# Performance work log

Hardware: AMD Instinct MI355X
Metric: run time of the kernel (lower is better)

The kernel has to match this reference:

```python
import jax, jax.numpy as jnp
import numpy as np

B, S, D, H, F = 8, 1024, 1024, 16, 4096
DH = D // H
EPS = 1e-8
NEG_INF = -1e30


def setup_inputs() -> dict:
    key = jax.random.key(0)
    ks = jax.random.split(key, 12)
    x = jax.random.normal(ks[0], (B, S, D), jnp.float32)
    # variable valid lengths in [S//2, S]; True = keep (valid token)
    lengths = jax.random.randint(ks[1], (B,), S // 2, S + 1)
    src_key_padding_mask = jnp.arange(S)[None, :] < lengths[:, None]
    rel_pos_bias = 0.02 * jax.random.normal(ks[2], (1, H, S, S), jnp.float32)
    w = lambda k, sh, std: std * jax.random.normal(k, sh, jnp.float32)
    std = D ** -0.5
    return {
        'x': x,
        'src_key_padding_mask': src_key_padding_mask,
        'rel_pos_bias': rel_pos_bias,
        'Wq': w(ks[3], (D, D), std),
        'Wk': w(ks[4], (D, D), std),
        'Wv': w(ks[5], (D, D), std),
        'Wo': w(ks[6], (D, D), std),
        'g1': jnp.ones((D,), jnp.float32),
        'g2': jnp.ones((D,), jnp.float32),
        'W1': w(ks[7], (D, F), std),
        'b1': jnp.zeros((F,), jnp.float32),
        'W2': w(ks[8], (F, F and D), F ** -0.5),
        'b2': jnp.zeros((D,), jnp.float32),
    }


def rmsnorm(x, g):
    # x / sqrt(mean(x^2) + eps) * g   (no mean subtraction)
    ms = jnp.mean(x * x, axis=-1, keepdims=True)
    return x * jax.lax.rsqrt(ms + EPS) * g


def attention(h, kpm, rel_pos_bias, Wq, Wk, Wv, Wo):
    b, s, d = h.shape
    q = (h @ Wq).reshape(b, s, H, DH)
    k = (h @ Wk).reshape(b, s, H, DH)
    v = (h @ Wv).reshape(b, s, H, DH)
    scores = jnp.einsum('bqhd,bkhd->bhqk', q, k) / np.sqrt(DH)
    scores = scores + rel_pos_bias
    scores = jnp.where(kpm[:, None, None, :], scores, NEG_INF)
    attn = jax.nn.softmax(scores, axis=-1)
    out = jnp.einsum('bhqk,bkhd->bqhd', attn, v).reshape(b, s, d)
    return out @ Wo


def reference(x, src_key_padding_mask, rel_pos_bias,
              Wq, Wk, Wv, Wo, g1, g2, W1, b1, W2, b2):
    h = rmsnorm(x, g1)
    x = x + attention(h, src_key_padding_mask, rel_pos_bias, Wq, Wk, Wv, Wo)
    h = rmsnorm(x, g2)
    ff = jax.nn.relu(h @ W1 + b1) @ W2 + b2
    return x + ff
```

## Files before the change

kernel.cpp:

```cpp
#include <hip/hip_runtime.h>
#include <stdint.h>

typedef __bf16 bf16;
typedef __bf16 bf16x4 __attribute__((ext_vector_type(4)));
typedef __bf16 bf16x8 __attribute__((ext_vector_type(8)));
typedef float f32x4 __attribute__((ext_vector_type(4)));

constexpr int Bz = 8, S = 1024, D = 1024, NH = 16, DH = 64, F = 4096;

__device__ __forceinline__ bool is_f32(const uint16_t* dt) { return dt[0] == 0; }

__device__ __forceinline__ void ld4(const void* p, size_t idx, bool f32, float o[4]) {
  if (f32) {
    float4 v = *(const float4*)((const float*)p + idx);
    o[0] = v.x; o[1] = v.y; o[2] = v.z; o[3] = v.w;
  } else {
    bf16x4 v = *(const bf16x4*)((const bf16*)p + idx);
    o[0] = v[0]; o[1] = v[1]; o[2] = v[2]; o[3] = v[3];
  }
}

__device__ __forceinline__ float ld1(const void* p, size_t idx, bool f32) {
  return f32 ? ((const float*)p)[idx] : (float)((const bf16*)p)[idx];
}

__device__ __forceinline__ void gload_lds16(const bf16* g, bf16* l) {
  __builtin_amdgcn_global_load_lds(
      (const __attribute__((address_space(1))) void*)g,
      (__attribute__((address_space(3))) void*)l, 16, 0, 0);
}

__global__ void lengths_kernel(const unsigned char* __restrict__ mask,
                               int* __restrict__ lengths) {
  int b = blockIdx.x;
  int esz = (mask[1] == 1) ? 1 : ((mask[1] != 0) ? 2 : 4);
  int cnt = 0;
  for (int s = threadIdx.x; s < S; s += blockDim.x) {
    const unsigned char* p = mask + ((size_t)b * S + s) * esz;
    unsigned v = 0;
    for (int j = 0; j < esz; j++) v |= p[j];
    cnt += (v != 0) ? 1 : 0;
  }
#pragma unroll
  for (int m = 32; m >= 1; m >>= 1) cnt += __shfl_xor(cnt, m);
  __shared__ int sred[4];
  if ((threadIdx.x & 63) == 0) sred[threadIdx.x >> 6] = cnt;
  __syncthreads();
  if (threadIdx.x == 0) lengths[b] = sred[0] + sred[1] + sred[2] + sred[3];
}

__global__ void transpose_any(const void* __restrict__ src, bf16* __restrict__ dst,
                              int R, int C, const uint16_t* __restrict__ dt) {
  bool f32 = is_f32(dt);
  __shared__ bf16 tile[64][65];
  int c0 = blockIdx.x * 64, r0 = blockIdx.y * 64;
  int tx = threadIdx.x, ty = threadIdx.y;
#pragma unroll
  for (int i = 0; i < 4; i++) {
    int r = ty * 4 + i;
    float v[4];
    ld4(src, (size_t)(r0 + r) * C + c0 + tx * 4, f32, v);
#pragma unroll
    for (int j = 0; j < 4; j++) tile[r][tx * 4 + j] = (bf16)v[j];
  }
  __syncthreads();
#pragma unroll
  for (int i = 0; i < 4; i++) {
    int rr = ty * 4 + i;
    bf16x4 ov;
#pragma unroll
    for (int j = 0; j < 4; j++) ov[j] = tile[tx * 4 + j][rr];
    *(bf16x4*)(dst + (size_t)(c0 + rr) * R + r0 + tx * 4) = ov;
  }
}

__global__ void bias_cvt(const void* __restrict__ src, bf16* __restrict__ dst,
                         const uint16_t* __restrict__ dt) {
  bool f32 = is_f32(dt);
  size_t i = ((size_t)blockIdx.x * 256 + threadIdx.x) * 4;
  float v[4];
  ld4(src, i, f32, v);
  bf16x4 o;
#pragma unroll
  for (int j = 0; j < 4; j++) o[j] = (bf16)(v[j] * 1.4426950408889634f);
  *(bf16x4*)(dst + i) = o;
}

template <bool ADD>
__global__ void rmsnorm_kernel(const void* __restrict__ xv, const bf16* __restrict__ add,
                               const void* __restrict__ gv, bf16* __restrict__ y,
                               const uint16_t* __restrict__ dt) {
  bool f32 = is_f32(dt);
  int row = blockIdx.x, t = threadIdx.x;
  float xf[4];
  ld4(xv, (size_t)row * D + t * 4, f32, xf);
  if (ADD) {
    bf16x4 a = *(const bf16x4*)(add + (size_t)row * D + t * 4);
#pragma unroll
    for (int j = 0; j < 4; j++) xf[j] += (float)a[j];
  }
  float ss = xf[0] * xf[0] + xf[1] * xf[1] + xf[2] * xf[2] + xf[3] * xf[3];
#pragma unroll
  for (int m = 32; m >= 1; m >>= 1) ss += __shfl_xor(ss, m);
  __shared__ float sred[4];
  if ((t & 63) == 0) sred[t >> 6] = ss;
  __syncthreads();
  float tot = sred[0] + sred[1] + sred[2] + sred[3];
  float scale = rsqrtf(tot * (1.0f / D) + 1e-8f);
  float gf[4];
  ld4(gv, (size_t)t * 4, f32, gf);
  bf16x4 ov;
#pragma unroll
  for (int j = 0; j < 4; j++) ov[j] = (bf16)(xf[j] * scale * gf[j]);
  *(bf16x4*)(y + (size_t)row * D + t * 4) = ov;
}

template <bool BIAS, bool RELU, bool RES1, bool RES2, bool OUTEXT, bool VT>
__global__ void gemm_nt(const bf16* __restrict__ A, const bf16* __restrict__ Bt,
                        void* __restrict__ Cv, const void* __restrict__ biasv,
                        const void* __restrict__ res1, const bf16* __restrict__ res2,
                        int M, int N, int K, const uint16_t* __restrict__ dt) {
  bool f32 = is_f32(dt);
  __shared__ bf16 As[2 * 4096];
  __shared__ bf16 Bs[2 * 4096];
  const int tid = threadIdx.x, lane = tid & 63, w = tid >> 6;
  const int wm = w >> 1, wn = w & 1;
  const int lid = blockIdx.x;
  const int bm = ((lid & 7) << 3) + ((lid >> 3) & 7);
  const int bn = lid >> 6;
  const int quad = lane >> 4, c = lane & 15;

  f32x4 acc[4][4];
#pragma unroll
  for (int i = 0; i < 4; i++)
#pragma unroll
    for (int j = 0; j < 4; j++)
#pragma unroll
      for (int r = 0; r < 4; r++) acc[i][j][r] = 0.f;

  const bf16* gA = A + (size_t)(bm * 128 + w * 16 + (lane >> 2)) * K + (lane & 3) * 8;
  const bf16* gB = Bt + (size_t)(bn * 128 + w * 16 + (lane >> 2)) * K + (lane & 3) * 8;
  bf16* lA = As + w * 512;
  bf16* lB = Bs + w * 512;
  const size_t rstep = (size_t)64 * K;

  int aoff[4], boff[4];
#pragma unroll
  for (int i = 0; i < 4; i++) {
    aoff[i] = (wm * 64 + i * 16 + c) * 32 + quad * 8;
    boff[i] = (wn * 64 + i * 16 + c) * 32 + quad * 8;
  }

  for (int k0 = 0; k0 < K; k0 += 64) {
    __syncthreads();
#pragma unroll
    for (int p = 0; p < 2; p++) {
      gload_lds16(gA + p * 32, lA + p * 4096);
      gload_lds16(gA + p * 32 + rstep, lA + p * 4096 + 2048);
      gload_lds16(gB + p * 32, lB + p * 4096);
      gload_lds16(gB + p * 32 + rstep, lB + p * 4096 + 2048);
    }
    gA += 64;
    gB += 64;
    __syncthreads();
#pragma unroll
    for (int p = 0; p < 2; p++) {
      bf16x8 af[4], bfr[4];
#pragma unroll
      for (int i = 0; i < 4; i++) af[i] = *(const bf16x8*)(As + p * 4096 + aoff[i]);
#pragma unroll
      for (int i = 0; i < 4; i++) bfr[i] = *(const bf16x8*)(Bs + p * 4096 + boff[i]);
#pragma unroll
      for (int i = 0; i < 4; i++)
#pragma unroll
        for (int j = 0; j < 4; j++)
          acc[i][j] = __builtin_amdgcn_mfma_f32_16x16x32_bf16(af[i], bfr[j], acc[i][j], 0, 0, 0);
    }
  }

  const int m0 = bm * 128 + wm * 64, n0 = bn * 128 + wn * 64;
#pragma unroll
  for (int i = 0; i < 4; i++) {
#pragma unroll
    for (int j = 0; j < 4; j++) {
      int col = n0 + j * 16 + c;
      if (VT) {
        int row0 = m0 + i * 16 + quad * 4;
        int bb = row0 >> 10, s0 = row0 & 1023;
        int hh = col >> 6, dd = col & 63;
        bf16x4 ov;
#pragma unroll
        for (int r = 0; r < 4; r++) ov[r] = (bf16)acc[i][j][r];
        *(bf16x4*)((bf16*)Cv + ((size_t)((bb << 4) + hh) * 64 + dd) * 1024 + s0) = ov;
      } else {
        float bv = BIAS ? ld1(biasv, col, f32) : 0.f;
#pragma unroll
        for (int r = 0; r < 4; r++) {
          int row = m0 + i * 16 + quad * 4 + r;
          size_t idx = (size_t)row * N + col;
          float vv = acc[i][j][r] + bv;
          if (RELU) vv = fmaxf(vv, 0.f);
          if (RES1) vv += ld1(res1, idx, f32);
          if (RES2) vv += (float)res2[idx];
          if (OUTEXT && f32) ((float*)Cv)[idx] = vv;
          else ((bf16*)Cv)[idx] = (bf16)vv;
        }
      }
    }
  }
}

#define SYNC()                            \
  do {                                    \
    __builtin_amdgcn_sched_barrier(0);    \
    __builtin_amdgcn_s_barrier();         \
    __builtin_amdgcn_sched_barrier(0);    \
  } while (0)
#define VMW(n)                                              \
  do {                                                      \
    asm volatile("s_waitcnt vmcnt(" #n ")" ::: "memory");   \
    __builtin_amdgcn_sched_barrier(0);                      \
  } while (0)
#define STA_(nb, rowbase, kb)                                                  \
  do {                                                                         \
    gload_lds16(Ag + (size_t)(rowbase) * K + (kb), &Abuf[nb][(rowbase) * 64]); \
    gload_lds16(Ag + (size_t)((rowbase) + 8) * K + (kb),                       \
                &Abuf[nb][((rowbase) + 8) * 64]);                              \
  } while (0)
#define STB_(nb, rowbase, kb)                                                  \
  do {                                                                         \
    gload_lds16(Bg + (size_t)(rowbase) * K + (kb), &Bbuf[nb][(rowbase) * 64]); \
    gload_lds16(Bg + (size_t)((rowbase) + 8) * K + (kb),                       \
                &Bbuf[nb][((rowbase) + 8) * 64]);                              \
  } while (0)
#define RDA_(MQ, fr, bufsel)                                                        \
  do {                                                                              \
    _Pragma("unroll") for (int ii = 0; ii < 4; ii++) {                              \
      int arow = wm * 128 + ((MQ)*4 + ii) * 16 + c;                                 \
      fr[ii][0] = *(const bf16x8*)&Abuf[bufsel][arow * 64 + ((quad ^ sx) * 8)];     \
      fr[ii][1] = *(const bf16x8*)&Abuf[bufsel][arow * 64 + (((4 + quad) ^ sx) * 8)]; \
    }                                                                               \
  } while (0)
#define RDB_(NQ, fr, bufsel)                                                        \
  do {                                                                              \
    _Pragma("unroll") for (int jj = 0; jj < 2; jj++) {                              \
      int brow = wn * 64 + ((NQ)*2 + jj) * 16 + c;                                  \
      fr[jj][0] = *(const bf16x8*)&Bbuf[bufsel][brow * 64 + ((quad ^ sx) * 8)];     \
      fr[jj][1] = *(const bf16x8*)&Bbuf[bufsel][brow * 64 + (((4 + quad) ^ sx) * 8)]; \
    }                                                                               \
  } while (0)

template <int MQ, int NQ>
__device__ __forceinline__ void mm_phase(f32x4 (&acc)[8][4], const bf16x8 (&afr)[4][2],
                                         const bf16x8 (&bfr)[2][2]) {
#pragma unroll
  for (int ii = 0; ii < 4; ii++)
#pragma unroll
    for (int jj = 0; jj < 2; jj++) {
      acc[MQ * 4 + ii][NQ * 2 + jj] = __builtin_amdgcn_mfma_f32_16x16x32_bf16(
          afr[ii][0], bfr[jj][0], acc[MQ * 4 + ii][NQ * 2 + jj], 0, 0, 0);
      acc[MQ * 4 + ii][NQ * 2 + jj] = __builtin_amdgcn_mfma_f32_16x16x32_bf16(
          afr[ii][1], bfr[jj][1], acc[MQ * 4 + ii][NQ * 2 + jj], 0, 0, 0);
    }
}

template <bool BIAS, bool RELU>
__global__ void __launch_bounds__(512, 2) gemm256(
    const bf16* __restrict__ A, const bf16* __restrict__ Bt, bf16* __restrict__ C,
    const void* __restrict__ biasv, int N, int K, const uint16_t* __restrict__ dt) {
  bool f32 = is_f32(dt);
  __shared__ bf16 Abuf[2][256 * 64];
  __shared__ bf16 Bbuf[2][256 * 64];
  const int tid = threadIdx.x, lane = tid & 63, w = tid >> 6;
  const int wm = w >> 2, wn = w & 3;
  const int quad = lane >> 4, c = lane & 15;
  const int sx = c & 7;
  const int nbn = N >> 8;
  const int nwg = gridDim.x;
  const int sid = (blockIdx.x & 7) * (nwg >> 3) + (blockIdx.x >> 3);
  const int bm = sid / nbn, bn = sid % nbn;

  const int lrow = lane >> 3;
  const int lslot = ((lane & 7) ^ lrow) * 8;
  const bf16* Ag = A + (size_t)(bm * 256 + lrow) * K + lslot;
  const bf16* Bg = Bt + (size_t)(bn * 256 + lrow) * K + lslot;

  const int ra0 = wm * 128 + wn * 16;
  const int ra1 = ra0 + 64;
  const int rb0 = (wn >> 1) * 128 + (wn & 1) * 64 + wm * 16;
  const int rb1 = rb0 + 32;

  f32x4 acc[8][4];
#pragma unroll
  for (int i = 0; i < 8; i++)
#pragma unroll
    for (int j = 0; j < 4; j++)
#pragma unroll
      for (int r = 0; r < 4; r++) acc[i][j][r] = 0.f;

  const int nt = K >> 6;

  STA_(0, ra0, 0);
  STA_(0, ra1, 0);
  STB_(0, rb0, 0);
  STB_(0, rb1, 0);
  STA_(1, ra0, 64);
  VMW(2);
  SYNC();

  for (int t = 0; t < nt; ++t) {
    const int buf = t & 1, nb = buf ^ 1;
    const int kb1 = (t + 1) << 6, kb2 = (t + 2) << 6;
    const bool st1 = (t + 1 < nt), st2 = (t + 2 < nt);
    bf16x8 afr[4][2], bfr0[2][2], bfr1[2][2];
    RDA_(0, afr, buf);
    RDB_(0, bfr0, buf);
    if (st1) STA_(nb, ra1, kb1);
    SYNC();
    __builtin_amdgcn_s_setprio(1);
    mm_phase<0, 0>(acc, afr, bfr0);
    __builtin_amdgcn_s_setprio(0);
    VMW(2);
    SYNC();
    RDB_(1, bfr1, buf);
    if (st1) STB_(nb, rb0, kb1);
    SYNC();
    __builtin_amdgcn_s_setprio(1);
    mm_phase<0, 1>(acc, afr, bfr1);
    __builtin_amdgcn_s_setprio(0);
    SYNC();
    RDA_(1, afr, buf);
    if (st2) STA_(buf, ra0, kb2);
    SYNC();
    __builtin_amdgcn_s_setprio(1);
    mm_phase<1, 0>(acc, afr, bfr0);
    __builtin_amdgcn_s_setprio(0);
    SYNC();
    if (st1) STB_(nb, rb1, kb1);
    SYNC();
    __builtin_amdgcn_s_setprio(1);
    mm_phase<1, 1>(acc, afr, bfr1);
    __builtin_amdgcn_s_setprio(0);
    VMW(4);
    SYNC();
  }

  const int m0 = bm * 256 + wm * 128, n0 = bn * 256 + wn * 64;
#pragma unroll
  for (int fi = 0; fi < 8; fi++)
#pragma unroll
    for (int fj = 0; fj < 4; fj++) {
      int col = n0 + fj * 16 + c;
      float bv = BIAS ? ld1(biasv, col, f32) : 0.f;
#pragma unroll
      for (int r = 0; r < 4; r++) {
        int row = m0 + fi * 16 + quad * 4 + r;
        float vv = acc[fi][fj][r] + bv;
        if (RELU) vv = fmaxf(vv, 0.f);
        C[(size_t)row * N + col] = (bf16)vv;
      }
    }
}

__global__ void __launch_bounds__(256) attn_kernel(
    const bf16* __restrict__ qk, const bf16* __restrict__ vt,
    const bf16* __restrict__ bias, const int* __restrict__ lengths,
    bf16* __restrict__ out) {
  __shared__ bf16 QPs[64 * 72];
  __shared__ bf16 Ks[64][72];
  __shared__ bf16 Vs[64][72];
  const int tid = threadIdx.x, lane = tid & 63, w = tid >> 6;
  const int id = blockIdx.x;
  const int qt = id >> 7, b = (id >> 4) & 7, h = id & 15;
  const int len = lengths[b];
  const int quad = lane >> 4, c = lane & 15;
  const int r4 = tid >> 2, c4 = tid & 3;

  {
    size_t qrow = (size_t)(b * S + qt * 64 + r4) * 2048 + h * 64 + c4 * 8;
    *(bf16x8*)&QPs[r4 * 72 + c4 * 8] = *(const bf16x8*)&qk[qrow];
    *(bf16x8*)&QPs[r4 * 72 + 32 + c4 * 8] = *(const bf16x8*)&qk[qrow + 32];
  }
  __syncthreads();
  const bf16x8 a0 = *(const bf16x8*)&QPs[(w * 16 + c) * 72 + quad * 8];
  const bf16x8 a1 = *(const bf16x8*)&QPs[(w * 16 + c) * 72 + 32 + quad * 8];

  bf16* Pw = QPs + w * 16 * 72;
  const int xsw = (quad & 2) << 3;
  const int xsr = (c & 8) << 1;

  float l_[4] = {0.f, 0.f, 0.f, 0.f};
  f32x4 o[4];
#pragma unroll
  for (int ni = 0; ni < 4; ni++)
#pragma unroll
    for (int r = 0; r < 4; r++) o[ni][r] = 0.f;

  const bf16* bbp = bias + (size_t)h * S * S + (size_t)(qt * 64 + w * 16 + quad * 4) * S;
  const int nkt = (len + 63) >> 6;

  const size_t KSTEP = (size_t)64 * 2048;
  const bf16* gk = qk + (size_t)(b * S + r4) * 2048 + 1024 + h * 64 + c4 * 8;
  const bf16* gv = vt + ((size_t)((b * 16 + h) * 64 + r4)) * 1024 + c4 * 8;
  bf16x8 kr0 = *(const bf16x8*)gk;
  bf16x8 kr1 = *(const bf16x8*)(gk + 32);
  bf16x8 vr0 = *(const bf16x8*)gv;
  bf16x8 vr1 = *(const bf16x8*)(gv + 32);
  gk += KSTEP;
  gv += 64;

  for (int kt = 0; kt < nkt; kt++) {
    __syncthreads();
    *(bf16x8*)&Ks[r4][c4 * 8] = kr0;
    *(bf16x8*)&Ks[r4][32 + c4 * 8] = kr1;
    *(bf16x8*)&Vs[r4][c4 * 8] = vr0;
    *(bf16x8*)&Vs[r4][32 + c4 * 8] = vr1;
    __syncthreads();

    bf16 br[4][4];
#pragma unroll
    for (int ni = 0; ni < 4; ni++)
#pragma unroll
      for (int r = 0; r < 4; r++) br[ni][r] = bbp[(size_t)r * S + ni * 16 + c];

    if (kt + 1 < nkt) {
      kr0 = *(const bf16x8*)gk;
      kr1 = *(const bf16x8*)(gk + 32);
      vr0 = *(const bf16x8*)gv;
      vr1 = *(const bf16x8*)(gv + 32);
      gk += KSTEP;
      gv += 64;
    }

    f32x4 s[4];
#pragma unroll
    for (int ni = 0; ni < 4; ni++)
#pragma unroll
      for (int r = 0; r < 4; r++) s[ni][r] = 0.f;
#pragma unroll
    for (int ni = 0; ni < 4; ni++) {
      bf16x8 b0 = *(const bf16x8*)&Ks[ni * 16 + c][quad * 8];
      bf16x8 b1 = *(const bf16x8*)&Ks[ni * 16 + c][32 + quad * 8];
      s[ni] = __builtin_amdgcn_mfma_f32_16x16x32_bf16(a0, b0, s[ni], 0, 0, 0);
      s[ni] = __builtin_amdgcn_mfma_f32_16x16x32_bf16(a1, b1, s[ni], 0, 0, 0);
    }

    const bool full = (kt * 64 + 64 <= len);
#pragma unroll
    for (int ni = 0; ni < 4; ni++) {
      int col = kt * 64 + ni * 16 + c;
      bool valid = full || (col < len);
#pragma unroll
      for (int r = 0; r < 4; r++) {
        float p = valid ? exp2f(fmaf(s[ni][r], 0.18033688011112042f, (float)br[ni][r])) : 0.f;
        s[ni][r] = p;
        l_[r] += p;
      }
    }

#pragma unroll
    for (int ni = 0; ni < 4; ni++)
#pragma unroll
      for (int r = 0; r < 4; r++)
        Pw[(quad * 4 + r) * 72 + ((ni * 16 + c) ^ xsw)] = (bf16)s[ni][r];

    bf16x8 p0 = *(const bf16x8*)&Pw[c * 72 + ((quad * 8) ^ xsr)];
    bf16x8 p1 = *(const bf16x8*)&Pw[c * 72 + ((32 + quad * 8) ^ xsr)];
#pragma unroll
    for (int ni = 0; ni < 4; ni++) {
      bf16x8 vb0 = *(const bf16x8*)&Vs[ni * 16 + c][quad * 8];
      bf16x8 vb1 = *(const bf16x8*)&Vs[ni * 16 + c][32 + quad * 8];
      o[ni] = __builtin_amdgcn_mfma_f32_16x16x32_bf16(p0, vb0, o[ni], 0, 0, 0);
      o[ni] = __builtin_amdgcn_mfma_f32_16x16x32_bf16(p1, vb1, o[ni], 0, 0, 0);
    }
    bbp += 64;
  }

  float inv[4];
#pragma unroll
  for (int r = 0; r < 4; r++) {
    float l = l_[r];
    l += __shfl_xor(l, 1);
    l += __shfl_xor(l, 2);
    l += __shfl_xor(l, 4);
    l += __shfl_xor(l, 8);
    inv[r] = 1.f / l;
  }
#pragma unroll
  for (int ni = 0; ni < 4; ni++)
#pragma unroll
    for (int r = 0; r < 4; r++) {
      size_t idx = ((size_t)(b * S + qt * 64 + w * 16 + quad * 4 + r)) * D + h * 64 + ni * 16 + c;
      out[idx] = (bf16)(o[ni][r] * inv[r]);
    }
}

extern "C" void kernel_launch(void* const* d_in, const int* in_sizes, int n_in,
                              void* d_out, int out_size, void* d_ws, size_t ws_size,
                              hipStream_t stream) {
  const void* x = d_in[0];
  const unsigned char* mask = (const unsigned char*)d_in[1];
  const void* rpb = d_in[2];
  const void* Wq = d_in[3];
  const void* Wk = d_in[4];
  const void* Wv = d_in[5];
  const void* Wo = d_in[6];
  const void* g1 = d_in[7];
  const void* g2 = d_in[8];
  const void* W1 = d_in[9];
  const void* b1 = d_in[10];
  const void* W2 = d_in[11];
  const void* b2 = d_in[12];
  const uint16_t* dt = (const uint16_t*)d_in[7];

  char* ws = (char*)d_ws;
  const size_t MB = 1024 * 1024;
  bf16* WqkT = (bf16*)(ws + 0 * MB);
  bf16* WkT = (bf16*)(ws + 2 * MB);
  bf16* WvT = (bf16*)(ws + 4 * MB);
  bf16* WoT = (bf16*)(ws + 6 * MB);
  bf16* W1T = (bf16*)(ws + 8 * MB);
  bf16* W2T = (bf16*)(ws + 16 * MB);
  bf16* hbuf = (bf16*)(ws + 24 * MB);
  bf16* qkbuf = (bf16*)(ws + 40 * MB);
  bf16* d1buf = (bf16*)(ws + 40 * MB);
  bf16* vtbuf = (bf16*)(ws + 72 * MB);
  bf16* biasb = (bf16*)(ws + 88 * MB);
  bf16* a1b = (bf16*)(ws + 56 * MB);
  int* lens = (int*)d_out;

  dim3 tb(16, 16);
  lengths_kernel<<<dim3(8), dim3(256), 0, stream>>>(mask, lens);
  transpose_any<<<dim3(16, 16), tb, 0, stream>>>(Wq, WqkT, 1024, 1024, dt);
  transpose_any<<<dim3(16, 16), tb, 0, stream>>>(Wk, WkT, 1024, 1024, dt);
  transpose_any<<<dim3(16, 16), tb, 0, stream>>>(Wv, WvT, 1024, 1024, dt);
  transpose_any<<<dim3(16, 16), tb, 0, stream>>>(Wo, WoT, 1024, 1024, dt);
  transpose_any<<<dim3(64, 16), tb, 0, stream>>>(W1, W1T, 1024, 4096, dt);
  transpose_any<<<dim3(16, 64), tb, 0, stream>>>(W2, W2T, 4096, 1024, dt);
  bias_cvt<<<dim3(16384), dim3(256), 0, stream>>>(rpb, biasb, dt);

  rmsnorm_kernel<false><<<dim3(8192), dim3(256), 0, stream>>>(x, nullptr, g1, hbuf, dt);
  gemm256<false, false><<<dim3(256), dim3(512), 0, stream>>>(
      hbuf, WqkT, qkbuf, nullptr, 2048, 1024, dt);
  gemm_nt<false, false, false, false, false, true><<<dim3(8 * 64), dim3(256), 0, stream>>>(
      hbuf, WvT, vtbuf, nullptr, nullptr, nullptr, 8192, 1024, 1024, dt);
  attn_kernel<<<dim3(2048), dim3(256), 0, stream>>>(qkbuf, vtbuf, biasb, lens, hbuf);
  gemm_nt<false, false, false, false, false, false><<<dim3(8 * 64), dim3(256), 0, stream>>>(
      hbuf, WoT, d1buf, nullptr, nullptr, nullptr, 8192, 1024, 1024, dt);
  rmsnorm_kernel<true><<<dim3(8192), dim3(256), 0, stream>>>(x, d1buf, g2, hbuf, dt);
  gemm256<true, true><<<dim3(512), dim3(512), 0, stream>>>(
      hbuf, W1T, a1b, b1, 4096, 1024, dt);
  gemm_nt<true, false, true, true, true, false><<<dim3(8 * 64), dim3(256), 0, stream>>>(
      a1b, W2T, d_out, b2, x, d1buf, 8192, 1024, 4096, dt);

  (void)in_sizes; (void)n_in; (void)out_size; (void)ws_size;
}
```

Before: 547.5 us.

## Deepen GEMM prefetch and add 256x128 tile kernel for Wo and W2 GEMMs

Restructures the 256x256 GEMM so each stage issues all four prefetch loads two tiles ahead instead of splitting loads across the current and next-next buffers, waiting on vmcnt(8) to keep more global loads in flight. Adds a new 256x128-tile, 8-wave GEMM with fused bias/relu/residual epilogue that uses the same LDS-direct prefetch scheme, and routes the Wo projection and the W2 FFN down-projection to it in place of the older gemm_nt kernel. The aim is better latency hiding and higher MFMA utilization on the N=1024 GEMMs. The cost is more in-flight loads and tighter barrier ordering, which could stall or race if the waitcnt accounting is wrong.

```diff
diff --git a/kernel.cpp b/kernel.cpp
--- a/kernel.cpp
+++ b/kernel.cpp
@@ -221,6 +221,9 @@
     asm volatile("s_waitcnt vmcnt(" #n ")" ::: "memory");   \
     __builtin_amdgcn_sched_barrier(0);                      \
   } while (0)
+#define PRIO1 __builtin_amdgcn_s_setprio(1)
+#define PRIO0 __builtin_amdgcn_s_setprio(0)
+
 #define STA_(nb, rowbase, kb)                                                  \
   do {                                                                         \
     gload_lds16(Ag + (size_t)(rowbase) * K + (kb), &Abuf[nb][(rowbase) * 64]); \
@@ -233,21 +236,21 @@
     gload_lds16(Bg + (size_t)((rowbase) + 8) * K + (kb),                       \
                 &Bbuf[nb][((rowbase) + 8) * 64]);                              \
   } while (0)
-#define RDA_(MQ, fr, bufsel)                                                        \
-  do {                                                                              \
-    _Pragma("unroll") for (int ii = 0; ii < 4; ii++) {                              \
-      int arow = wm * 128 + ((MQ)*4 + ii) * 16 + c;                                 \
-      fr[ii][0] = *(const bf16x8*)&Abuf[bufsel][arow * 64 + ((quad ^ sx) * 8)];     \
+#define RDA_(MQ, fr, bufsel)                                                          \
+  do {                                                                                \
+    _Pragma("unroll") for (int ii = 0; ii < 4; ii++) {                                \
+      int arow = wm * 128 + ((MQ)*4 + ii) * 16 + c;                                   \
+      fr[ii][0] = *(const bf16x8*)&Abuf[bufsel][arow * 64 + ((quad ^ sx) * 8)];       \
       fr[ii][1] = *(const bf16x8*)&Abuf[bufsel][arow * 64 + (((4 + quad) ^ sx) * 8)]; \
-    }                                                                               \
-  } while (0)
-#define RDB_(NQ, fr, bufsel)                                                        \
-  do {                                                                              \
-    _Pragma("unroll") for (int jj = 0; jj < 2; jj++) {                              \
-      int brow = wn * 64 + ((NQ)*2 + jj) * 16 + c;                                  \
-      fr[jj][0] = *(const bf16x8*)&Bbuf[bufsel][brow * 64 + ((quad ^ sx) * 8)];     \
+    }                                                                                 \
+  } while (0)
+#define RDB_(NQ, fr, bufsel)                                                          \
+  do {                                                                                \
+    _Pragma("unroll") for (int jj = 0; jj < 2; jj++) {                                \
+      int brow = wn * 64 + ((NQ)*2 + jj) * 16 + c;                                    \
+      fr[jj][0] = *(const bf16x8*)&Bbuf[bufsel][brow * 64 + ((quad ^ sx) * 8)];       \
       fr[jj][1] = *(const bf16x8*)&Bbuf[bufsel][brow * 64 + (((4 + quad) ^ sx) * 8)]; \
-    }                                                                               \
+    }                                                                                 \
   } while (0)
 
 template <int MQ, int NQ>
@@ -265,7 +268,7 @@
 }
 
 template <bool BIAS, bool RELU>
-__global__ void __launch_bounds__(512, 2) gemm256(
+__global__ void __launch_bounds__(512, 2) gemm256d(
     const bf16* __restrict__ A, const bf16* __restrict__ Bt, bf16* __restrict__ C,
     const void* __restrict__ biasv, int N, int K, const uint16_t* __restrict__ dt) {
   bool f32 = is_f32(dt);
@@ -305,43 +308,51 @@
   STB_(0, rb0, 0);
   STB_(0, rb1, 0);
   STA_(1, ra0, 64);
-  VMW(2);
+  STA_(1, ra1, 64);
+  STB_(1, rb0, 64);
+  STB_(1, rb1, 64);
+  VMW(8);
   SYNC();
 
   for (int t = 0; t < nt; ++t) {
-    const int buf = t & 1, nb = buf ^ 1;
-    const int kb1 = (t + 1) << 6, kb2 = (t + 2) << 6;
-    const bool st1 = (t + 1 < nt), st2 = (t + 2 < nt);
+    const int buf = t & 1;
+    const int kb2 = (t + 2) << 6;
+    const bool st2 = (t + 2 < nt);
     bf16x8 afr[4][2], bfr0[2][2], bfr1[2][2];
     RDA_(0, afr, buf);
     RDB_(0, bfr0, buf);
-    if (st1) STA_(nb, ra1, kb1);
-    SYNC();
-    __builtin_amdgcn_s_setprio(1);
+    SYNC();
+    PRIO1;
     mm_phase<0, 0>(acc, afr, bfr0);
-    __builtin_amdgcn_s_setprio(0);
-    VMW(2);
+    PRIO0;
     SYNC();
     RDB_(1, bfr1, buf);
-    if (st1) STB_(nb, rb0, kb1);
-    SYNC();
-    __builtin_amdgcn_s_setprio(1);
+    if (st2) {
+      STA_(buf, ra0, kb2);
+      STB_(buf, rb0, kb2);
+    }
+    SYNC();
+    PRIO1;
     mm_phase<0, 1>(acc, afr, bfr1);
-    __builtin_amdgcn_s_setprio(0);
+    PRIO0;
     SYNC();
     RDA_(1, afr, buf);
-    if (st2) STA_(buf, ra0, kb2);
-    SYNC();
-    __builtin_amdgcn_s_setprio(1);
+    if (st2) STB_(buf, rb1, kb2);
+    SYNC();
+    PRIO1;
     mm_phase<1, 0>(acc, afr, bfr0);
-    __builtin_amdgcn_s_setprio(0);
-    SYNC();
-    if (st1) STB_(nb, rb1, kb1);
-    SYNC();
-    __builtin_amdgcn_s_setprio(1);
+    PRIO0;
+    SYNC();
+    if (st2) STA_(buf, ra1, kb2);
+    SYNC();
+    PRIO1;
     mm_phase<1, 1>(acc, afr, bfr1);
-    __builtin_amdgcn_s_setprio(0);
-    VMW(4);
+    PRIO0;
+    if (st2) {
+      VMW(8);
+    } else {
+      VMW(0);
+    }
     SYNC();
   }
 
@@ -358,6 +369,154 @@
         float vv = acc[fi][fj][r] + bv;
         if (RELU) vv = fmaxf(vv, 0.f);
         C[(size_t)row * N + col] = (bf16)vv;
+      }
+    }
+}
+
+#define NSTA(nb, kb)                                                             \
+  do {                                                                           \
+    gload_lds16(Ag + (size_t)(aw) * K + (kb), &Abuf[nb][(aw)*64]);               \
+    gload_lds16(Ag + (size_t)(aw + 8) * K + (kb), &Abuf[nb][(aw + 8) * 64]);     \
+    gload_lds16(Ag + (size_t)(aw + 16) * K + (kb), &Abuf[nb][(aw + 16) * 64]);   \
+    gload_lds16(Ag + (size_t)(aw + 24) * K + (kb), &Abuf[nb][(aw + 24) * 64]);   \
+  } while (0)
+#define NSTB(nb, kb)                                                             \
+  do {                                                                           \
+    gload_lds16(Bg + (size_t)(bw) * K + (kb), &Bbuf[nb][(bw)*64]);               \
+    gload_lds16(Bg + (size_t)(bw + 8) * K + (kb), &Bbuf[nb][(bw + 8) * 64]);     \
+  } while (0)
+#define NRDA(KH, fr)                                                                         \
+  do {                                                                                       \
+    _Pragma("unroll") for (int mi = 0; mi < 4; mi++) fr[mi] =                                \
+        *(const bf16x8*)&Abuf[buf][(wm * 64 + mi * 16 + c) * 64 + ((((KH)*4 + quad) ^ sx) * 8)]; \
+  } while (0)
+#define NRDB(NJH, KH, fr)                                                                    \
+  do {                                                                                       \
+    _Pragma("unroll") for (int j = 0; j < 2; j++) fr[j] =                                    \
+        *(const bf16x8*)&Bbuf[buf][(wn * 64 + ((NJH)*2 + j) * 16 + c) * 64 +                 \
+                                   ((((KH)*4 + quad) ^ sx) * 8)];                            \
+  } while (0)
+
+template <int NJH>
+__device__ __forceinline__ void mm8(f32x4 (&acc)[4][4], const bf16x8 (&af)[4],
+                                    const bf16x8 (&bf_)[2]) {
+#pragma unroll
+  for (int mi = 0; mi < 4; mi++)
+#pragma unroll
+    for (int j = 0; j < 2; j++)
+      acc[mi][NJH * 2 + j] = __builtin_amdgcn_mfma_f32_16x16x32_bf16(
+          af[mi], bf_[j], acc[mi][NJH * 2 + j], 0, 0, 0);
+}
+
+template <bool BIAS, bool RELU, bool RES1, bool RES2, bool OUTEXT>
+__global__ void __launch_bounds__(512, 2) gemm256n(
+    const bf16* __restrict__ A, const bf16* __restrict__ Bt, void* __restrict__ Cv,
+    const void* __restrict__ biasv, const void* __restrict__ res1,
+    const bf16* __restrict__ res2, int N, int K, const uint16_t* __restrict__ dt) {
+  bool f32 = is_f32(dt);
+  __shared__ bf16 Abuf[2][256 * 64];
+  __shared__ bf16 Bbuf[2][128 * 64];
+  const int tid = threadIdx.x, lane = tid & 63, w = tid >> 6;
+  const int wm = w >> 1, wn = w & 1;
+  const int quad = lane >> 4, c = lane & 15;
+  const int sx = c & 7;
+  const int nbn = N >> 7;
+  const int nwg = gridDim.x;
+  const int sid = (blockIdx.x & 7) * (nwg >> 3) + (blockIdx.x >> 3);
+  const int bm = sid / nbn, bn = sid % nbn;
+
+  const int lrow = lane >> 3;
+  const int lslot = ((lane & 7) ^ lrow) * 8;
+  const bf16* Ag = A + (size_t)(bm * 256 + lrow) * K + lslot;
+  const bf16* Bg = Bt + (size_t)(bn * 128 + lrow) * K + lslot;
+  const int aw = w * 32, bw = w * 16;
+  const bool wlate = (w & 2) != 0;
+
+  f32x4 acc[4][4];
+#pragma unroll
+  for (int i = 0; i < 4; i++)
+#pragma unroll
+    for (int j = 0; j < 4; j++)
+#pragma unroll
+      for (int r = 0; r < 4; r++) acc[i][j][r] = 0.f;
+
+  const int nt = K >> 6;
+
+  NSTA(0, 0);
+  NSTB(0, 0);
+  NSTA(1, 64);
+  if (!wlate) NSTB(1, 64);
+  if (wlate) {
+    VMW(4);
+  } else {
+    VMW(6);
+  }
+  SYNC();
+
+  for (int t = 0; t < nt; ++t) {
+    const int buf = t & 1, nb = buf ^ 1;
+    const int kb1 = (t + 1) << 6, kb2 = (t + 2) << 6;
+    const bool st1 = (t + 1 < nt), st2 = (t + 2 < nt);
+    bf16x8 af[4], bf_[2];
+    NRDA(0, af);
+    NRDB(0, 0, bf_);
+    if (wlate && st1) NSTB(nb, kb1);
+    SYNC();
+    PRIO1;
+    mm8<0>(acc, af, bf_);
+    PRIO0;
+    SYNC();
+    NRDB(1, 0, bf_);
+    SYNC();
+    PRIO1;
+    mm8<1>(acc, af, bf_);
+    PRIO0;
+    SYNC();
+    NRDA(1, af);
+    NRDB(0, 1, bf_);
+    SYNC();
+    PRIO1;
+    mm8<0>(acc, af, bf_);
+    PRIO0;
+    SYNC();
+    NRDB(1, 1, bf_);
+    if (st2) {
+      NSTA(buf, kb2);
+      if (!wlate) NSTB(buf, kb2);
+    }
+    SYNC();
+    PRIO1;
+    mm8<1>(acc, af, bf_);
+    PRIO0;
+    if (st2) {
+      if (wlate) {
+        VMW(4);
+      } else {
+        VMW(6);
+      }
+    } else {
+      VMW(0);
+    }
+    SYNC();
+  }
+
+  const int m0 = bm * 256 + wm * 64, n0 = bn * 128 + wn * 64;
+#pragma unroll
+  for (int mi = 0; mi < 4; mi++)
+#pragma unroll
+    for (int nj = 0; nj < 4; nj++) {
+      int col = n0 + nj * 16 + c;
+      float bv = BIAS ? ld1(biasv, col, f32) : 0.f;
+#pragma unroll
+      for (int r = 0; r < 4; r++) {
+        int row = m0 + mi * 16 + quad * 4 + r;
+        size_t idx = (size_t)row * N + col;
+        float vv = acc[mi][nj][r] + bv;
+        if (RELU) vv = fmaxf(vv, 0.f);
+        if (RES1) vv += ld1(res1, idx, f32);
+        if (RES2) vv += (float)res2[idx];
+        if (OUTEXT && f32) ((float*)Cv)[idx] = vv;
+        else ((bf16*)Cv)[idx] = (bf16)vv;
       }
     }
 }
@@ -540,18 +699,18 @@
   bias_cvt<<<dim3(16384), dim3(256), 0, stream>>>(rpb, biasb, dt);
 
   rmsnorm_kernel<false><<<dim3(8192), dim3(256), 0, stream>>>(x, nullptr, g1, hbuf, dt);
-  gemm256<false, false><<<dim3(256), dim3(512), 0, stream>>>(
+  gemm256d<false, false><<<dim3(256), dim3(512), 0, stream>>>(
       hbuf, WqkT, qkbuf, nullptr, 2048, 1024, dt);
   gemm_nt<false, false, false, false, false, true><<<dim3(8 * 64), dim3(256), 0, stream>>>(
       hbuf, WvT, vtbuf, nullptr, nullptr, nullptr, 8192, 1024, 1024, dt);
   attn_kernel<<<dim3(2048), dim3(256), 0, stream>>>(qkbuf, vtbuf, biasb, lens, hbuf);
-  gemm_nt<false, false, false, false, false, false><<<dim3(8 * 64), dim3(256), 0, stream>>>(
-      hbuf, WoT, d1buf, nullptr, nullptr, nullptr, 8192, 1024, 1024, dt);
+  gemm256n<false, false, false, false, false><<<dim3(256), dim3(512), 0, stream>>>(
+      hbuf, WoT, d1buf, nullptr, nullptr, nullptr, 1024, 1024, dt);
   rmsnorm_kernel<true><<<dim3(8192), dim3(256), 0, stream>>>(x, d1buf, g2, hbuf, dt);
-  gemm256<true, true><<<dim3(512), dim3(512), 0, stream>>>(
+  gemm256d<true, true><<<dim3(512), dim3(512), 0, stream>>>(
       hbuf, W1T, a1b, b1, 4096, 1024, dt);
-  gemm_nt<true, false, true, true, true, false><<<dim3(8 * 64), dim3(256), 0, stream>>>(
-      a1b, W2T, d_out, b2, x, d1buf, 8192, 1024, 4096, dt);
+  gemm256n<true, false, true, true, true><<<dim3(256), dim3(512), 0, stream>>>(
+      a1b, W2T, d_out, b2, x, d1buf, 1024, 4096, dt);
 
   (void)in_sizes; (void)n_in; (void)out_size; (void)ws_size;
 }
```

After: 560.5 us. 2.4% more time.

## Fuse V projection into QK gemm and merge weight prep launches

Applied to the files above, without the earlier changes.

The V projection now runs in the same 256x256 gemm as Q and K by widening N to 3072. Tiles in the V column range write a transposed per-head layout straight from the accumulators. The six weight transposes and the bias conversion are merged into a single prep kernel that dispatches on block index. This cuts the number of kernel launches and swaps the smaller-tile V gemm for the larger-tile kernel, at the cost of strided bf16x4 scatter stores for the V part.

```diff
diff --git a/kernel.cpp b/kernel.cpp
--- a/kernel.cpp
+++ b/kernel.cpp
@@ -49,12 +49,44 @@
   if (threadIdx.x == 0) lengths[b] = sred[0] + sred[1] + sred[2] + sred[3];
 }
 
-__global__ void transpose_any(const void* __restrict__ src, bf16* __restrict__ dst,
-                              int R, int C, const uint16_t* __restrict__ dt) {
+__global__ void prep_all(const void* __restrict__ sq, const void* __restrict__ sk,
+                         const void* __restrict__ sv, const void* __restrict__ so,
+                         const void* __restrict__ s1, const void* __restrict__ s2,
+                         bf16* __restrict__ dq, bf16* __restrict__ dk,
+                         bf16* __restrict__ dv, bf16* __restrict__ do_,
+                         bf16* __restrict__ d1, bf16* __restrict__ d2,
+                         const void* __restrict__ rpb, bf16* __restrict__ biasb,
+                         const uint16_t* __restrict__ dt) {
   bool f32 = is_f32(dt);
+  int t = blockIdx.x;
+  int tx = threadIdx.x, ty = threadIdx.y;
+  if (t >= 3072) {
+    size_t i = ((size_t)(t - 3072) * 256 + ty * 16 + tx) * 4;
+    float v[4];
+    ld4(rpb, i, f32, v);
+    bf16x4 o;
+#pragma unroll
+    for (int j = 0; j < 4; j++) o[j] = (bf16)(v[j] * 1.4426950408889634f);
+    *(bf16x4*)(biasb + i) = o;
+    return;
+  }
+  const void* src;
+  bf16* dst;
+  int R, C, gx, base;
+  if (t < 1024) {
+    int wsel = t >> 8;
+    base = wsel << 8;
+    src = wsel == 0 ? sq : wsel == 1 ? sk : wsel == 2 ? sv : so;
+    dst = wsel == 0 ? dq : wsel == 1 ? dk : wsel == 2 ? dv : do_;
+    R = 1024; C = 1024; gx = 16;
+  } else if (t < 2048) {
+    base = 1024; src = s1; dst = d1; R = 1024; C = 4096; gx = 64;
+  } else {
+    base = 2048; src = s2; dst = d2; R = 4096; C = 1024; gx = 16;
+  }
+  int rel = t - base;
+  int c0 = (rel % gx) * 64, r0 = (rel / gx) * 64;
   __shared__ bf16 tile[64][65];
-  int c0 = blockIdx.x * 64, r0 = blockIdx.y * 64;
-  int tx = threadIdx.x, ty = threadIdx.y;
 #pragma unroll
   for (int i = 0; i < 4; i++) {
     int r = ty * 4 + i;
@@ -72,18 +104,6 @@
     for (int j = 0; j < 4; j++) ov[j] = tile[tx * 4 + j][rr];
     *(bf16x4*)(dst + (size_t)(c0 + rr) * R + r0 + tx * 4) = ov;
   }
-}
-
-__global__ void bias_cvt(const void* __restrict__ src, bf16* __restrict__ dst,
-                         const uint16_t* __restrict__ dt) {
-  bool f32 = is_f32(dt);
-  size_t i = ((size_t)blockIdx.x * 256 + threadIdx.x) * 4;
-  float v[4];
-  ld4(src, i, f32, v);
-  bf16x4 o;
-#pragma unroll
-  for (int j = 0; j < 4; j++) o[j] = (bf16)(v[j] * 1.4426950408889634f);
-  *(bf16x4*)(dst + i) = o;
 }
 
 template <bool ADD>
@@ -221,6 +241,7 @@
     asm volatile("s_waitcnt vmcnt(" #n ")" ::: "memory");   \
     __builtin_amdgcn_sched_barrier(0);                      \
   } while (0)
+
 #define STA_(nb, rowbase, kb)                                                  \
   do {                                                                         \
     gload_lds16(Ag + (size_t)(rowbase) * K + (kb), &Abuf[nb][(rowbase) * 64]); \
@@ -233,21 +254,21 @@
     gload_lds16(Bg + (size_t)((rowbase) + 8) * K + (kb),                       \
                 &Bbuf[nb][((rowbase) + 8) * 64]);                              \
   } while (0)
-#define RDA_(MQ, fr, bufsel)                                                        \
-  do {                                                                              \
-    _Pragma("unroll") for (int ii = 0; ii < 4; ii++) {                              \
-      int arow = wm * 128 + ((MQ)*4 + ii) * 16 + c;                                 \
-      fr[ii][0] = *(const bf16x8*)&Abuf[bufsel][arow * 64 + ((quad ^ sx) * 8)];     \
+#define RDA_(MQ, fr, bufsel)                                                          \
+  do {                                                                                \
+    _Pragma("unroll") for (int ii = 0; ii < 4; ii++) {                                \
+      int arow = wm * 128 + ((MQ)*4 + ii) * 16 + c;                                   \
+      fr[ii][0] = *(const bf16x8*)&Abuf[bufsel][arow * 64 + ((quad ^ sx) * 8)];       \
       fr[ii][1] = *(const bf16x8*)&Abuf[bufsel][arow * 64 + (((4 + quad) ^ sx) * 8)]; \
-    }                                                                               \
+    }                                                                                 \
   } while (0)
-#define RDB_(NQ, fr, bufsel)                                                        \
-  do {                                                                              \
-    _Pragma("unroll") for (int jj = 0; jj < 2; jj++) {                              \
-      int brow = wn * 64 + ((NQ)*2 + jj) * 16 + c;                                  \
-      fr[jj][0] = *(const bf16x8*)&Bbuf[bufsel][brow * 64 + ((quad ^ sx) * 8)];     \
+#define RDB_(NQ, fr, bufsel)                                                          \
+  do {                                                                                \
+    _Pragma("unroll") for (int jj = 0; jj < 2; jj++) {                                \
+      int brow = wn * 64 + ((NQ)*2 + jj) * 16 + c;                                    \
+      fr[jj][0] = *(const bf16x8*)&Bbuf[bufsel][brow * 64 + ((quad ^ sx) * 8)];       \
       fr[jj][1] = *(const bf16x8*)&Bbuf[bufsel][brow * 64 + (((4 + quad) ^ sx) * 8)]; \
-    }                                                                               \
+    }                                                                                 \
   } while (0)
 
 template <int MQ, int NQ>
@@ -264,10 +285,11 @@
     }
 }
 
-template <bool BIAS, bool RELU>
+template <bool BIAS, bool RELU, bool QKV>
 __global__ void __launch_bounds__(512, 2) gemm256(
     const bf16* __restrict__ A, const bf16* __restrict__ Bt, bf16* __restrict__ C,
-    const void* __restrict__ biasv, int N, int K, const uint16_t* __restrict__ dt) {
+    bf16* __restrict__ C2, const void* __restrict__ biasv, int N, int K,
+    const uint16_t* __restrict__ dt) {
   bool f32 = is_f32(dt);
   __shared__ bf16 Abuf[2][256 * 64];
   __shared__ bf16 Bbuf[2][256 * 64];
@@ -346,6 +368,23 @@
   }
 
   const int m0 = bm * 256 + wm * 128, n0 = bn * 256 + wn * 64;
+  if (QKV && n0 >= 2048) {
+#pragma unroll
+    for (int fi = 0; fi < 8; fi++)
+#pragma unroll
+      for (int fj = 0; fj < 4; fj++) {
+        int vcol = n0 + fj * 16 + c - 2048;
+        int hh = vcol >> 6, dd = vcol & 63;
+        int row0 = m0 + fi * 16 + quad * 4;
+        int bb = row0 >> 10, s0 = row0 & 1023;
+        bf16x4 ov;
+#pragma unroll
+        for (int r = 0; r < 4; r++) ov[r] = (bf16)acc[fi][fj][r];
+        *(bf16x4*)(C2 + ((size_t)((bb << 4) + hh) * 64 + dd) * 1024 + s0) = ov;
+      }
+    return;
+  }
+  const int ldc = QKV ? 2048 : N;
 #pragma unroll
   for (int fi = 0; fi < 8; fi++)
 #pragma unroll
@@ -357,7 +396,7 @@
         int row = m0 + fi * 16 + quad * 4 + r;
         float vv = acc[fi][fj][r] + bv;
         if (RELU) vv = fmaxf(vv, 0.f);
-        C[(size_t)row * N + col] = (bf16)vv;
+        C[(size_t)row * ldc + col] = (bf16)vv;
       }
     }
 }
@@ -529,27 +568,19 @@
   bf16* a1b = (bf16*)(ws + 56 * MB);
   int* lens = (int*)d_out;
 
-  dim3 tb(16, 16);
   lengths_kernel<<<dim3(8), dim3(256), 0, stream>>>(mask, lens);
-  transpose_any<<<dim3(16, 16), tb, 0, stream>>>(Wq, WqkT, 1024, 1024, dt);
-  transpose_any<<<dim3(16, 16), tb, 0, stream>>>(Wk, WkT, 1024, 1024, dt);
-  transpose_any<<<dim3(16, 16), tb, 0, stream>>>(Wv, WvT, 1024, 1024, dt);
-  transpose_any<<<dim3(16, 16), tb, 0, stream>>>(Wo, WoT, 1024, 1024, dt);
-  transpose_any<<<dim3(64, 16), tb, 0, stream>>>(W1, W1T, 1024, 4096, dt);
-  transpose_any<<<dim3(16, 64), tb, 0, stream>>>(W2, W2T, 4096, 1024, dt);
-  bias_cvt<<<dim3(16384), dim3(256), 0, stream>>>(rpb, biasb, dt);
+  prep_all<<<dim3(3072 + 16384), dim3(16, 16), 0, stream>>>(
+      Wq, Wk, Wv, Wo, W1, W2, WqkT, WkT, WvT, WoT, W1T, W2T, rpb, biasb, dt);
 
   rmsnorm_kernel<false><<<dim3(8192), dim3(256), 0, stream>>>(x, nullptr, g1, hbuf, dt);
-  gemm256<false, false><<<dim3(256), dim3(512), 0, stream>>>(
-      hbuf, WqkT, qkbuf, nullptr, 2048, 1024, dt);
-  gemm_nt<false, false, false, false, false, true><<<dim3(8 * 64), dim3(256), 0, stream>>>(
-      hbuf, WvT, vtbuf, nullptr, nullptr, nullptr, 8192, 1024, 1024, dt);
+  gemm256<false, false, true><<<dim3(384), dim3(512), 0, stream>>>(
+      hbuf, WqkT, qkbuf, vtbuf, nullptr, 3072, 1024, dt);
   attn_kernel<<<dim3(2048), dim3(256), 0, stream>>>(qkbuf, vtbuf, biasb, lens, hbuf);
   gemm_nt<false, false, false, false, false, false><<<dim3(8 * 64), dim3(256), 0, stream>>>(
       hbuf, WoT, d1buf, nullptr, nullptr, nullptr, 8192, 1024, 1024, dt);
   rmsnorm_kernel<true><<<dim3(8192), dim3(256), 0, stream>>>(x, d1buf, g2, hbuf, dt);
-  gemm256<true, true><<<dim3(512), dim3(512), 0, stream>>>(
-      hbuf, W1T, a1b, b1, 4096, 1024, dt);
+  gemm256<true, true, false><<<dim3(512), dim3(512), 0, stream>>>(
+      hbuf, W1T, a1b, nullptr, b1, 4096, 1024, dt);
   gemm_nt<true, false, true, true, true, false><<<dim3(8 * 64), dim3(256), 0, stream>>>(
       a1b, W2T, d_out, b2, x, d1buf, 8192, 1024, 4096, dt);
 
```

Result: no change. 536.9 us (-1.9%).
